# Performance work log

Hardware: AMD Instinct MI355X
Metric: run time of the kernel (lower is better)

The kernel has to match this reference:

```python
import jax, jax.numpy as jnp
import numpy as np

NUM_GRAPHS = 2048


def gcn_conv(x, W, b, edge, N):
    # PyG GCNConv: x' = D^{-1/2} (A + I) D^{-1/2} (x W) + b
    src, dst = edge[0], edge[1]
    loop = jnp.arange(N, dtype=src.dtype)
    src = jnp.concatenate([src, loop])
    dst = jnp.concatenate([dst, loop])
    h = x @ W  # [N, out]
    deg = jax.ops.segment_sum(jnp.ones(dst.shape, x.dtype), dst, num_segments=N)
    dinv = jnp.where(deg > 0, jax.lax.rsqrt(deg), 0.0)
    norm = dinv[src] * dinv[dst]  # [E+N]
    out = jax.ops.segment_sum(h[src] * norm[:, None], dst, num_segments=N)
    return out + b


def pool_max_mean(x, batch, G):
    mx = jax.ops.segment_max(x, batch, num_segments=G)
    mx = jnp.where(jnp.isfinite(mx), mx, 0.0)  # guard empty segments
    s = jax.ops.segment_sum(x, batch, num_segments=G)
    cnt = jax.ops.segment_sum(jnp.ones((x.shape[0],), x.dtype), batch, num_segments=G)
    mean = s / jnp.maximum(cnt, 1.0)[:, None]
    return mx, mean


def setup_inputs() -> dict:
    key = jax.random.key(0)
    ks = jax.random.split(key, 20)
    F, CE, SE, DD = 64, 64, 32, 128
    Nc, Ec, Ns, Es = 100000, 1250000, 100000, 1250000

    def glorot(k, shape):
        fan_in, fan_out = shape[0], shape[1]
        lim = np.sqrt(6.0 / (fan_in + fan_out)).astype(np.float32)
        return jax.random.uniform(k, shape, jnp.float32, -lim, lim)

    inp = {
        "c": jax.random.normal(ks[0], (Nc, F), jnp.float32),
        "c_edge": jax.random.randint(ks[1], (2, Ec), 0, Nc),
        "c_batch": jnp.sort(jax.random.randint(ks[2], (Nc,), 0, NUM_GRAPHS)),
        "s": jax.random.normal(ks[3], (Ns, F), jnp.float32),
        "s_edge": jax.random.randint(ks[4], (2, Es), 0, Ns),
        "s_batch": jnp.sort(jax.random.randint(ks[5], (Ns,), 0, NUM_GRAPHS)),
        "Wc0": glorot(ks[6], (F, CE)), "bc0": jnp.zeros((CE,), jnp.float32),
        "Wc1": glorot(ks[7], (CE, CE)), "bc1": jnp.zeros((CE,), jnp.float32),
        "Wc2": glorot(ks[8], (CE, CE)), "bc2": jnp.zeros((CE,), jnp.float32),
        "Ws0": glorot(ks[9], (F, SE)), "bs0": jnp.zeros((SE,), jnp.float32),
        "Ws1": glorot(ks[10], (SE, SE)), "bs1": jnp.zeros((SE,), jnp.float32),
        "Ws2": glorot(ks[11], (SE, SE)), "bs2": jnp.zeros((SE,), jnp.float32),
        "Wd": glorot(ks[12], ((CE + SE) * 2, DD)), "bd": jnp.zeros((DD,), jnp.float32),
        "Wo": glorot(ks[13], (DD, 1)), "bo": jnp.zeros((1,), jnp.float32),
    }
    return inp


def reference(c, c_edge, c_batch, s, s_edge, s_batch,
              Wc0, bc0, Wc1, bc1, Wc2, bc2,
              Ws0, bs0, Ws1, bs1, Ws2, bs2,
              Wd, bd, Wo, bo):
    Nc, Ns = c.shape[0], s.shape[0]
    cro = jax.nn.relu(gcn_conv(c, Wc0, bc0, c_edge, Nc))
    cro = jax.nn.relu(gcn_conv(cro, Wc1, bc1, c_edge, Nc))
    cro = jax.nn.relu(gcn_conv(cro, Wc2, bc2, c_edge, Nc))
    solv = jax.nn.relu(gcn_conv(s, Ws0, bs0, s_edge, Ns))
    solv = jax.nn.relu(gcn_conv(solv, Ws1, bs1, s_edge, Ns))
    solv = jax.nn.relu(gcn_conv(solv, Ws2, bs2, s_edge, Ns))
    c_mx, c_mean = pool_max_mean(cro, c_batch, NUM_GRAPHS)
    s_mx, s_mean = pool_max_mean(solv, s_batch, NUM_GRAPHS)
    embed = jnp.concatenate([c_mx, c_mean, s_mx, s_mean], axis=1)  # [G, 192]
    dense = jax.nn.relu(embed @ Wd + bd)
    out = dense @ Wo + bo  # [G, 1]
    return out, embed
```

## Files before the change

### kernel.cpp

```cpp
#include <hip/hip_runtime.h>
#include <hip/hip_fp16.h>
#include <math.h>


static inline int cdiv(int a, int b) { return (a + b - 1) / b; }

#define BUCKET_CAP 8192
#define P1_CHUNK   4096

typedef _Float16 v8h __attribute__((ext_vector_type(8)));
typedef float    v4f __attribute__((ext_vector_type(4)));

__global__ void zero_int(int* __restrict__ p, int n) {
    int i = blockIdx.x * blockDim.x + threadIdx.x;
    if (i < n) p[i] = 0;
}

__global__ __launch_bounds__(256) void p1_partition(const int* __restrict__ c_edge, int Ec,
                                                    const int* __restrict__ s_edge, int Es,
                                                    int Nc_pad, int Etot, int nbuck,
                                                    int* __restrict__ bucket_fill,
                                                    unsigned* __restrict__ pk) {
    __shared__ unsigned       wbuf[P1_CHUNK];
    __shared__ unsigned short bbuf[P1_CHUNK];
    __shared__ int            hist[512];
    int e0 = blockIdx.x * P1_CHUNK;
    int n  = Etot - e0;
    if (n > P1_CHUNK) n = P1_CHUNK;
    for (int i = threadIdx.x; i < nbuck; i += 256) hist[i] = 0;
    __syncthreads();
    for (int i = threadIdx.x; i < n; i += 256) {
        int e = e0 + i, src, g;
        if (e < Ec) { src = c_edge[e]; g = c_edge[Ec + e]; }
        else        { int e2 = e - Ec; src = s_edge[e2]; g = Nc_pad + s_edge[Es + e2]; }
        int b   = g >> 9;
        wbuf[i] = ((unsigned)(g & 511) << 17) | (unsigned)src;
        bbuf[i] = (unsigned short)b;
        atomicAdd(&hist[b], 1);
    }
    __syncthreads();
    for (int i = threadIdx.x; i < nbuck; i += 256) {
        int h = hist[i];
        hist[i] = h ? atomicAdd(&bucket_fill[i], h) : 0;
    }
    __syncthreads();
    for (int i = threadIdx.x; i < n; i += 256) {
        int b    = bbuf[i];
        int slot = atomicAdd(&hist[b], 1);
        if (slot < BUCKET_CAP) pk[(size_t)b * BUCKET_CAP + slot] = wbuf[i];
    }
}

__global__ __launch_bounds__(512) void p2_scanbuckets(const int* __restrict__ fill, int nbuck,
                                                      int* __restrict__ basearr,
                                                      int* __restrict__ off_all, int Ntot_pad, int Etot) {
    __shared__ int sh[512];
    int v = (threadIdx.x < nbuck) ? fill[threadIdx.x] : 0;
    sh[threadIdx.x] = v;
    __syncthreads();
    for (int ofs = 1; ofs < 512; ofs <<= 1) {
        int t = (threadIdx.x >= ofs) ? sh[threadIdx.x - ofs] : 0;
        __syncthreads();
        sh[threadIdx.x] += t;
        __syncthreads();
    }
    if (threadIdx.x < nbuck) basearr[threadIdx.x] = sh[threadIdx.x] - v;
    if (threadIdx.x == 0) off_all[Ntot_pad] = Etot;
}

__global__ __launch_bounds__(512) void p3_build(const unsigned* __restrict__ pk,
                                                const int* __restrict__ fillarr,
                                                const int* __restrict__ basearr,
                                                int* __restrict__ off_all,
                                                float* __restrict__ dinv,
                                                int* __restrict__ csr) {
    __shared__ int sh[512];
    int b    = blockIdx.x;
    int fill = fillarr[b];
    if (fill > BUCKET_CAP) fill = BUCKET_CAP;
    int base = basearr[b];
    const unsigned* reg = pk + (size_t)b * BUCKET_CAP;
    sh[threadIdx.x] = 0;
    __syncthreads();
    for (int i = threadIdx.x; i < fill; i += 512) atomicAdd(&sh[reg[i] >> 17], 1);
    __syncthreads();
    int cnt = sh[threadIdx.x];
    for (int ofs = 1; ofs < 512; ofs <<= 1) {
        int t = (threadIdx.x >= ofs) ? sh[threadIdx.x - ofs] : 0;
        __syncthreads();
        sh[threadIdx.x] += t;
        __syncthreads();
    }
    int excl = sh[threadIdx.x] - cnt;
    int node = b * 512 + threadIdx.x;
    off_all[node] = base + excl;
    dinv[node]    = rsqrtf((float)(cnt + 1));
    __syncthreads();
    sh[threadIdx.x] = excl;
    __syncthreads();
    for (int i = threadIdx.x; i < fill; i += 512) {
        unsigned w    = reg[i];
        int      slot = atomicAdd(&sh[w >> 17], 1);
        csr[base + slot] = (int)(w & 0x1FFFFu);
    }
}

template <int K, int M, typename TIN>
__device__ void gemm_mfma(int bid, const TIN* __restrict__ X, const float* __restrict__ W,
                          const float* __restrict__ dinv, __half* __restrict__ H, int N,
                          char* smem_) {
    constexpr int RB = 64;
    constexpr int KP = K + 8;
    constexpr int NT = M / 16;
    constexpr int KS = K / 32;
    _Float16* Xh = (_Float16*)smem_;
    _Float16* Wz = Xh + RB * KP;
    const int t    = threadIdx.x;
    const int row0 = bid * RB;

    constexpr int WENT = NT * KS * 64;
    for (int idx = t; idx < WENT; idx += 256) {
        int lane = idx & 63, rest = idx >> 6;
        int ks = rest % KS, ntl = rest / KS;
        int kbase = ks * 32 + (lane >> 4) * 8;
        int col   = ntl * 16 + (lane & 15);
        union { float4 f4; _Float16 h[8]; } u;
#pragma unroll
        for (int j = 0; j < 8; ++j) u.h[j] = (_Float16)W[(kbase + j) * M + col];
        *(float4*)(Wz + idx * 8) = u.f4;
    }
    if constexpr (sizeof(TIN) == 4) {
        constexpr int NI = RB * K / 4;
        for (int idx = t; idx < NI; idx += 256) {
            int row = idx / (K / 4), k4 = idx % (K / 4);
            int gr = row0 + row;
            float4 v = make_float4(0.f, 0.f, 0.f, 0.f);
            if (gr < N) v = *(const float4*)((const float*)X + (size_t)gr * K + k4 * 4);
            union { float2 f2; _Float16 h[4]; } u;
            u.h[0] = (_Float16)v.x; u.h[1] = (_Float16)v.y;
            u.h[2] = (_Float16)v.z; u.h[3] = (_Float16)v.w;
            *(float2*)(Xh + row * KP + k4 * 4) = u.f2;
        }
    } else {
        constexpr int NI = RB * K / 8;
        for (int idx = t; idx < NI; idx += 256) {
            int row = idx / (K / 8), k8 = idx % (K / 8);
            int gr = row0 + row;
            float4 v = make_float4(0.f, 0.f, 0.f, 0.f);
            if (gr < N) v = *(const float4*)((const __half*)X + (size_t)gr * K + k8 * 8);
            *(float4*)(Xh + row * KP + k8 * 8) = v;
        }
    }
    __syncthreads();

    const int wave = t >> 6, lane = t & 63;
    const int quad = lane >> 4, nl = lane & 15;
    const int rowA = wave * 16 + nl;

    v4f acc[NT];
#pragma unroll
    for (int i = 0; i < NT; ++i) acc[i] = (v4f){0.f, 0.f, 0.f, 0.f};

#pragma unroll
    for (int ks = 0; ks < KS; ++ks) {
        v8h a = *(const v8h*)(Xh + rowA * KP + ks * 32 + quad * 8);
#pragma unroll
        for (int ntl = 0; ntl < NT; ++ntl) {
            v8h b = *(const v8h*)(Wz + ((ntl * KS + ks) * 64 + lane) * 8);
            acc[ntl] = __builtin_amdgcn_mfma_f32_16x16x32_f16(a, b, acc[ntl], 0, 0, 0);
        }
    }

#pragma unroll
    for (int r = 0; r < 4; ++r) {
        int gr = row0 + wave * 16 + quad * 4 + r;
        if (gr < N) {
            float dv = dinv[gr];
#pragma unroll
            for (int ntl = 0; ntl < NT; ++ntl)
                H[(size_t)gr * M + ntl * 16 + nl] = __float2half(acc[ntl][r] * dv);
        }
    }
}

__device__ __forceinline__ float4 load4h(const float2* __restrict__ base, size_t idx) {
    float2 r = base[idx];
    union { float2 f2; __half2 h2[2]; } u;
    u.f2 = r;
    float2 a = __half22float2(u.h2[0]);
    float2 b = __half22float2(u.h2[1]);
    return make_float4(a.x, a.y, b.x, b.y);
}

__device__ __forceinline__ void load8h(const float4* __restrict__ base, size_t idx,
                                       float* __restrict__ o) {
    float4 r = base[idx];
    union { float4 f4; __half2 h2[4]; } u;
    u.f4 = r;
    float2 p0 = __half22float2(u.h2[0]);
    float2 p1 = __half22float2(u.h2[1]);
    float2 p2 = __half22float2(u.h2[2]);
    float2 p3 = __half22float2(u.h2[3]);
    o[0] = p0.x; o[1] = p0.y; o[2] = p1.x; o[3] = p1.y;
    o[4] = p2.x; o[5] = p2.y; o[6] = p3.x; o[7] = p3.y;
}

template <int MF>
__device__ void fused_agg_gemm(int bid, const __half* __restrict__ Hin,
                               const int* __restrict__ off_g, const int* __restrict__ csr,
                               const float* __restrict__ dinv_g, const float* __restrict__ b,
                               const float* __restrict__ W, __half* __restrict__ Hout,
                               int N, char* smem_) {
    constexpr int KP = MF + 8;
    constexpr int NT = MF / 16;
    constexpr int KS = MF / 32;
    _Float16* Xh = (_Float16*)smem_;
    _Float16* Wz = Xh + 64 * KP;
    const int t = threadIdx.x;

    constexpr int WENT = NT * KS * 64;
    for (int idx = t; idx < WENT; idx += 256) {
        int lane = idx & 63, rest = idx >> 6;
        int ks = rest % KS, ntl = rest / KS;
        int kbase = ks * 32 + (lane >> 4) * 8;
        int col   = ntl * 16 + (lane & 15);
        union { float4 f4; _Float16 h[8]; } u;
#pragma unroll
        for (int j = 0; j < 8; ++j) u.h[j] = (_Float16)W[(kbase + j) * MF + col];
        *(float4*)(Wz + idx * 8) = u.f4;
    }

    constexpr int L      = MF / 8;
    constexpr int NPW    = 64 / L;
    constexpr int PASSES = 64 / (4 * NPW);
    const int lane = t & 63, wave = t >> 6;
    const int fq = lane & (L - 1), sub = lane / L;
    const float4* H4 = (const float4*)Hin;
    const float4* b4 = (const float4*)b;
    float bb[8];
    {
        float4 b0 = b4[fq * 2], b1 = b4[fq * 2 + 1];
        bb[0] = b0.x; bb[1] = b0.y; bb[2] = b0.z; bb[3] = b0.w;
        bb[4] = b1.x; bb[5] = b1.y; bb[6] = b1.z; bb[7] = b1.w;
    }
#pragma unroll
    for (int pass = 0; pass < PASSES; ++pass) {
        int ln   = (pass * 4 + wave) * NPW + sub;
        int node = bid * 64 + ln;
        if (node < N) {
            int j0 = off_g[node], j1 = off_g[node + 1];
            float acc[8];
            load8h(H4, (size_t)node * L + fq, acc);
            int j = j0;
            for (; j + 8 <= j1; j += 8) {
                int s0 = csr[j],     s1 = csr[j + 1], s2 = csr[j + 2], s3 = csr[j + 3];
                int s4 = csr[j + 4], s5 = csr[j + 5], s6 = csr[j + 6], s7 = csr[j + 7];
                float a0[8], a1[8], a2[8], a3[8], a4[8], a5[8], a6[8], a7[8];
                load8h(H4, (size_t)s0 * L + fq, a0);
                load8h(H4, (size_t)s1 * L + fq, a1);
                load8h(H4, (size_t)s2 * L + fq, a2);
                load8h(H4, (size_t)s3 * L + fq, a3);
                load8h(H4, (size_t)s4 * L + fq, a4);
                load8h(H4, (size_t)s5 * L + fq, a5);
                load8h(H4, (size_t)s6 * L + fq, a6);
                load8h(H4, (size_t)s7 * L + fq, a7);
#pragma unroll
                for (int f = 0; f < 8; ++f) {
                    float g1 = ((a0[f] + a1[f]) + a2[f]) + a3[f];
                    float g2 = ((a4[f] + a5[f]) + a6[f]) + a7[f];
                    acc[f] += g1 + g2;
                }
            }
            for (; j + 4 <= j1; j += 4) {
                int s0 = csr[j], s1 = csr[j + 1], s2 = csr[j + 2], s3 = csr[j + 3];
                float a0[8], a1[8], a2[8], a3[8];
                load8h(H4, (size_t)s0 * L + fq, a0);
                load8h(H4, (size_t)s1 * L + fq, a1);
                load8h(H4, (size_t)s2 * L + fq, a2);
                load8h(H4, (size_t)s3 * L + fq, a3);
#pragma unroll
                for (int f = 0; f < 8; ++f)
                    acc[f] += ((a0[f] + a1[f]) + a2[f]) + a3[f];
            }
            for (; j < j1; ++j) {
                float a0[8];
                load8h(H4, (size_t)csr[j] * L + fq, a0);
#pragma unroll
                for (int f = 0; f < 8; ++f) acc[f] += a0[f];
            }
            float dv = dinv_g[node];
            union { float4 f4; __half2 h2[4]; } o;
#pragma unroll
            for (int p2 = 0; p2 < 4; ++p2) {
                float vx = dv * acc[2 * p2]     + bb[2 * p2];
                float vy = dv * acc[2 * p2 + 1] + bb[2 * p2 + 1];
                o.h2[p2] = __floats2half2_rn(vx > 0.f ? vx : 0.f, vy > 0.f ? vy : 0.f);
            }
            *(float4*)(Xh + ln * KP + fq * 8) = o.f4;
        } else {
            *(float4*)(Xh + ln * KP + fq * 8) = make_float4(0.f, 0.f, 0.f, 0.f);
        }
    }
    __syncthreads();

    const int quad = lane >> 4, nl = lane & 15;
    const int rowA = wave * 16 + nl;
    v4f acc2[NT];
#pragma unroll
    for (int i = 0; i < NT; ++i) acc2[i] = (v4f){0.f, 0.f, 0.f, 0.f};
#pragma unroll
    for (int ks = 0; ks < KS; ++ks) {
        v8h av = *(const v8h*)(Xh + rowA * KP + ks * 32 + quad * 8);
#pragma unroll
        for (int ntl = 0; ntl < NT; ++ntl) {
            v8h bv = *(const v8h*)(Wz + ((ntl * KS + ks) * 64 + lane) * 8);
            acc2[ntl] = __builtin_amdgcn_mfma_f32_16x16x32_f16(av, bv, acc2[ntl], 0, 0, 0);
        }
    }
#pragma unroll
    for (int r = 0; r < 4; ++r) {
        int gr = bid * 64 + wave * 16 + quad * 4 + r;
        if (gr < N) {
            float dv = dinv_g[gr];
#pragma unroll
            for (int ntl = 0; ntl < NT; ++ntl)
                Hout[(size_t)gr * MF + ntl * 16 + nl] = __float2half(acc2[ntl][r] * dv);
        }
    }
}

template <int M>
__device__ void agg_body(int bid, const __half* __restrict__ H,
                         const int* __restrict__ off_g,
                         const int* __restrict__ csr,
                         const float* __restrict__ dinv_g,
                         const float* __restrict__ b,
                         __half* __restrict__ out, int Nloc) {
    constexpr int L   = M / 4;
    constexpr int NPW = 64 / L;
    int lane = threadIdx.x & 63;
    int wave = threadIdx.x >> 6;
    int fq   = lane & (L - 1);
    int sub  = lane / L;
    int node = (bid * 4 + wave) * NPW + sub;
    if (node >= Nloc) return;
    const float2* H4 = (const float2*)H;
    int j0 = off_g[node], j1 = off_g[node + 1];
    float4 acc = load4h(H4, (size_t)node * L + fq);
    int j = j0;
    for (; j + 8 <= j1; j += 8) {
        int s0 = csr[j],     s1 = csr[j + 1], s2 = csr[j + 2], s3 = csr[j + 3];
        int s4 = csr[j + 4], s5 = csr[j + 5], s6 = csr[j + 6], s7 = csr[j + 7];
        float4 a0 = load4h(H4, (size_t)s0 * L + fq);
        float4 a1 = load4h(H4, (size_t)s1 * L + fq);
        float4 a2 = load4h(H4, (size_t)s2 * L + fq);
        float4 a3 = load4h(H4, (size_t)s3 * L + fq);
        float4 a4 = load4h(H4, (size_t)s4 * L + fq);
        float4 a5 = load4h(H4, (size_t)s5 * L + fq);
        float4 a6 = load4h(H4, (size_t)s6 * L + fq);
        float4 a7 = load4h(H4, (size_t)s7 * L + fq);
        acc.x += (a0.x + a1.x + a2.x + a3.x) + (a4.x + a5.x + a6.x + a7.x);
        acc.y += (a0.y + a1.y + a2.y + a3.y) + (a4.y + a5.y + a6.y + a7.y);
        acc.z += (a0.z + a1.z + a2.z + a3.z) + (a4.z + a5.z + a6.z + a7.z);
        acc.w += (a0.w + a1.w + a2.w + a3.w) + (a4.w + a5.w + a6.w + a7.w);
    }
    for (; j + 4 <= j1; j += 4) {
        int s0 = csr[j], s1 = csr[j + 1], s2 = csr[j + 2], s3 = csr[j + 3];
        float4 a0 = load4h(H4, (size_t)s0 * L + fq);
        float4 a1 = load4h(H4, (size_t)s1 * L + fq);
        float4 a2 = load4h(H4, (size_t)s2 * L + fq);
        float4 a3 = load4h(H4, (size_t)s3 * L + fq);
        acc.x += a0.x + a1.x + a2.x + a3.x;
        acc.y += a0.y + a1.y + a2.y + a3.y;
        acc.z += a0.z + a1.z + a2.z + a3.z;
        acc.w += a0.w + a1.w + a2.w + a3.w;
    }
    for (; j < j1; ++j) {
        float4 a = load4h(H4, (size_t)csr[j] * L + fq);
        acc.x += a.x; acc.y += a.y; acc.z += a.z; acc.w += a.w;
    }
    float  dv = dinv_g[node];
    float4 bb = ((const float4*)b)[fq];
    float  vx = dv * acc.x + bb.x;
    float  vy = dv * acc.y + bb.y;
    float  vz = dv * acc.z + bb.z;
    float  vw = dv * acc.w + bb.w;
    union { float2 f2; __half2 h2[2]; } o;
    o.h2[0] = __floats2half2_rn(vx > 0.f ? vx : 0.f, vy > 0.f ? vy : 0.f);
    o.h2[1] = __floats2half2_rn(vz > 0.f ? vz : 0.f, vw > 0.f ? vw : 0.f);
    ((float2*)out)[(size_t)node * L + fq] = o.f2;
}

__global__ __launch_bounds__(256) void gemmBoth0(const float* __restrict__ Xc, const float* __restrict__ Wc,
                                                 __half* __restrict__ cH, int Nc,
                                                 const float* __restrict__ Xs, const float* __restrict__ Ws,
                                                 __half* __restrict__ sH, int Ns,
                                                 const float* __restrict__ dinv_all, int Nc_pad, int nbC) {
    __shared__ __align__(16) char smem[17408];
    if (blockIdx.x < nbC) gemm_mfma<64, 64, float>(blockIdx.x, Xc, Wc, dinv_all, cH, Nc, smem);
    else                  gemm_mfma<64, 32, float>(blockIdx.x - nbC, Xs, Ws, dinv_all + Nc_pad, sH, Ns, smem);
}

__global__ __launch_bounds__(256) void fusedBoth(
        const __half* __restrict__ cHin, __half* __restrict__ cHout,
        const float* __restrict__ Wc, const float* __restrict__ bc,
        const __half* __restrict__ sHin, __half* __restrict__ sHout,
        const float* __restrict__ Ws, const float* __restrict__ bs,
        const int* __restrict__ off_all, const int* __restrict__ csr_all,
        const float* __restrict__ dinv_all,
        int Nc, int Ns, int Nc_pad, int nbC) {
    __shared__ __align__(16) char smem[17408];
    if (blockIdx.x < nbC)
        fused_agg_gemm<64>(blockIdx.x, cHin, off_all, csr_all, dinv_all, bc, Wc, cHout, Nc, smem);
    else
        fused_agg_gemm<32>(blockIdx.x - nbC, sHin, off_all + Nc_pad, csr_all,
                           dinv_all + Nc_pad, bs, Ws, sHout, Ns, smem);
}

__global__ __launch_bounds__(256) void aggBoth(const __half* __restrict__ cH, const __half* __restrict__ sH,
                                               const int* __restrict__ off_all, const int* __restrict__ csr_all,
                                               const float* __restrict__ dinv_all,
                                               const float* __restrict__ bc, const float* __restrict__ bs,
                                               __half* __restrict__ outc, __half* __restrict__ outs,
                                               int Nc, int Ns, int Nc_pad, int nbC) {
    if (blockIdx.x < nbC)
        agg_body<64>(blockIdx.x, cH, off_all, csr_all, dinv_all, bc, outc, Nc);
    else
        agg_body<32>(blockIdx.x - nbC, sH, off_all + Nc_pad, csr_all,
                     dinv_all + Nc_pad, bs, outs, Ns);
}

__device__ __forceinline__ int lbound(const int* __restrict__ a, int n, int key) {
    int lo = 0, hi = n;
    while (lo < hi) {
        int mid = (lo + hi) >> 1;
        if (a[mid] < key) lo = mid + 1; else hi = mid;
    }
    return lo;
}

__global__ __launch_bounds__(256) void poolDense(const __half* __restrict__ cX, const int* __restrict__ c_batch, int Nc,
                                                 const __half* __restrict__ sX, const int* __restrict__ s_batch, int Ns,
                                                 const float* __restrict__ Wd, const float* __restrict__ bd,
                                                 const float* __restrict__ Wo, const float* __restrict__ bo,
                                                 float* __restrict__ outv, float* __restrict__ embed) {
    __shared__ float e[192];
    __shared__ float red[2048];
    __shared__ float rs[128];
    int g = blockIdx.x, t = threadIdx.x;
    const float2* c4 = (const float2*)cX;
    const float2* s4 = (const float2*)sX;
    int clo = lbound(c_batch, Nc, g), chi = lbound(c_batch, Nc, g + 1);
    {
        int q = t & 15, grp = t >> 4;
        float mx0 = 0.f, mx1 = 0.f, mx2 = 0.f, mx3 = 0.f;
        float sm0 = 0.f, sm1 = 0.f, sm2 = 0.f, sm3 = 0.f;
        for (int i = clo + grp; i < chi; i += 16) {
            float4 v = load4h(c4, (size_t)i * 16 + q);
            mx0 = fmaxf(mx0, v.x); sm0 += v.x;
            mx1 = fmaxf(mx1, v.y); sm1 += v.y;
            mx2 = fmaxf(mx2, v.z); sm2 += v.z;
            mx3 = fmaxf(mx3, v.w); sm3 += v.w;
        }
        red[grp * 64 + q * 4 + 0]        = mx0;
        red[grp * 64 + q * 4 + 1]        = mx1;
        red[grp * 64 + q * 4 + 2]        = mx2;
        red[grp * 64 + q * 4 + 3]        = mx3;
        red[1024 + grp * 64 + q * 4 + 0] = sm0;
        red[1024 + grp * 64 + q * 4 + 1] = sm1;
        red[1024 + grp * 64 + q * 4 + 2] = sm2;
        red[1024 + grp * 64 + q * 4 + 3] = sm3;
    }
    __syncthreads();
    if (t < 64) {
        float m = red[t], s = red[1024 + t];
#pragma unroll
        for (int grp = 1; grp < 16; ++grp) {
            m = fmaxf(m, red[grp * 64 + t]);
            s += red[1024 + grp * 64 + t];
        }
        int cn = chi - clo;
        e[t]      = m;
        e[64 + t] = s / (float)(cn > 0 ? cn : 1);
    }
    __syncthreads();
    int slo = lbound(s_batch, Ns, g), shi = lbound(s_batch, Ns, g + 1);
    {
        int q = t & 7, grp = t >> 3;
        float mx0 = 0.f, mx1 = 0.f, mx2 = 0.f, mx3 = 0.f;
        float sm0 = 0.f, sm1 = 0.f, sm2 = 0.f, sm3 = 0.f;
        for (int i = slo + grp; i < shi; i += 32) {
            float4 v = load4h(s4, (size_t)i * 8 + q);
            mx0 = fmaxf(mx0, v.x); sm0 += v.x;
            mx1 = fmaxf(mx1, v.y); sm1 += v.y;
            mx2 = fmaxf(mx2, v.z); sm2 += v.z;
            mx3 = fmaxf(mx3, v.w); sm3 += v.w;
        }
        red[grp * 32 + q * 4 + 0]        = mx0;
        red[grp * 32 + q * 4 + 1]        = mx1;
        red[grp * 32 + q * 4 + 2]        = mx2;
        red[grp * 32 + q * 4 + 3]        = mx3;
        red[1024 + grp * 32 + q * 4 + 0] = sm0;
        red[1024 + grp * 32 + q * 4 + 1] = sm1;
        red[1024 + grp * 32 + q * 4 + 2] = sm2;
        red[1024 + grp * 32 + q * 4 + 3] = sm3;
    }
    __syncthreads();
    if (t < 32) {
        float m = red[t], s = red[1024 + t];
#pragma unroll
        for (int grp = 1; grp < 32; ++grp) {
            m = fmaxf(m, red[grp * 32 + t]);
            s += red[1024 + grp * 32 + t];
        }
        int cn = shi - slo;
        e[128 + t] = m;
        e[160 + t] = s / (float)(cn > 0 ? cn : 1);
    }
    __syncthreads();
    if (t < 192) embed[(size_t)g * 192 + t] = e[t];
    if (t < 128) {
        float acc = bd[t];
        for (int k = 0; k < 192; ++k) acc += e[k] * Wd[k * 128 + t];
        float d = acc > 0.f ? acc : 0.f;
        rs[t] = d * Wo[t];
    }
    __syncthreads();
    for (int ofs = 64; ofs > 0; ofs >>= 1) {
        if (t < ofs) rs[t] += rs[t + ofs];
        __syncthreads();
    }
    if (t == 0) outv[g] = rs[0] + bo[0];
}


extern "C" void kernel_launch(void* const* d_in, const int* in_sizes, int n_in,
                              void* d_out, int out_size, void* d_ws, size_t ws_size,
                              hipStream_t stream) {
    const float* c       = (const float*)d_in[0];
    const int*   c_edge  = (const int*)d_in[1];
    const int*   c_batch = (const int*)d_in[2];
    const float* s       = (const float*)d_in[3];
    const int*   s_edge  = (const int*)d_in[4];
    const int*   s_batch = (const int*)d_in[5];
    const float* Wc0 = (const float*)d_in[6],  *bc0 = (const float*)d_in[7];
    const float* Wc1 = (const float*)d_in[8],  *bc1 = (const float*)d_in[9];
    const float* Wc2 = (const float*)d_in[10], *bc2 = (const float*)d_in[11];
    const float* Ws0 = (const float*)d_in[12], *bs0 = (const float*)d_in[13];
    const float* Ws1 = (const float*)d_in[14], *bs1 = (const float*)d_in[15];
    const float* Ws2 = (const float*)d_in[16], *bs2 = (const float*)d_in[17];
    const float* Wd  = (const float*)d_in[18], *bd  = (const float*)d_in[19];
    const float* Wo  = (const float*)d_in[20], *bo  = (const float*)d_in[21];

    const int Nc = in_sizes[0] / 64;
    const int Ec = in_sizes[1] / 2;
    const int Ns = in_sizes[3] / 64;
    const int Es = in_sizes[4] / 2;
    const int G  = out_size / 193;
    const int Nc_pad   = cdiv(Nc, 512) * 512;
    const int Ns_pad   = cdiv(Ns, 512) * 512;
    const int Ntot_pad = Nc_pad + Ns_pad;
    const int Etot     = Ec + Es;
    const int nbuck    = Ntot_pad >> 9;

    char* p = (char*)d_ws;
    auto  alloc = [&](size_t bytes) -> void* {
        void* r = (void*)p;
        p += (bytes + 255) & ~(size_t)255;
        return r;
    };
    int*      bucket_fill = (int*)alloc(512 * 4);
    int*      bucket_base = (int*)alloc(512 * 4);
    unsigned* pk          = (unsigned*)alloc((size_t)nbuck * BUCKET_CAP * 4);
    int*      off_all     = (int*)alloc(((size_t)Ntot_pad + 1) * 4);
    int*      csr_all     = (int*)alloc((size_t)Etot * 4);
    float*    dinv_all    = (float*)alloc((size_t)Ntot_pad * 4);
    __half*   bufC        = (__half*)alloc((size_t)Nc * 64 * 2);
    __half*   bufS        = (__half*)alloc((size_t)Ns * 32 * 2);
    __half*   cHa         = (__half*)alloc((size_t)Nc * 64 * 2);
    __half*   cHb         = (__half*)alloc((size_t)Nc * 64 * 2);
    __half*   sHa         = (__half*)alloc((size_t)Ns * 32 * 2);
    __half*   sHb         = (__half*)alloc((size_t)Ns * 32 * 2);

    float* outv  = (float*)d_out;
    float* embed = outv + G;

    const int nbGmC = cdiv(Nc, 64), nbGmS = cdiv(Ns, 64);
    const int nbFC  = cdiv(Nc, 64), nbFS  = cdiv(Ns, 64);
    const int nbAgC = Nc_pad / 16,  nbAgS = Ns_pad / 32;

    zero_int<<<cdiv(nbuck, 256), 256, 0, stream>>>(bucket_fill, nbuck);
    p1_partition<<<cdiv(Etot, P1_CHUNK), 256, 0, stream>>>(c_edge, Ec, s_edge, Es,
                                                           Nc_pad, Etot, nbuck, bucket_fill, pk);
    p2_scanbuckets<<<1, 512, 0, stream>>>(bucket_fill, nbuck, bucket_base, off_all, Ntot_pad, Etot);
    p3_build<<<nbuck, 512, 0, stream>>>(pk, bucket_fill, bucket_base,
                                        off_all, dinv_all, csr_all);

    gemmBoth0<<<nbGmC + nbGmS, 256, 0, stream>>>(c, Wc0, cHa, Nc, s, Ws0, sHa, Ns,
                                                 dinv_all, Nc_pad, nbGmC);

    fusedBoth<<<nbFC + nbFS, 256, 0, stream>>>(cHa, cHb, Wc1, bc0, sHa, sHb, Ws1, bs0,
                                               off_all, csr_all, dinv_all,
                                               Nc, Ns, Nc_pad, nbFC);
    fusedBoth<<<nbFC + nbFS, 256, 0, stream>>>(cHb, cHa, Wc2, bc1, sHb, sHa, Ws2, bs1,
                                               off_all, csr_all, dinv_all,
                                               Nc, Ns, Nc_pad, nbFC);

    aggBoth<<<nbAgC + nbAgS, 256, 0, stream>>>(cHa, sHa, off_all, csr_all, dinv_all,
                                               bc2, bs2, bufC, bufS, Nc, Ns, Nc_pad, nbAgC);

    poolDense<<<G, 256, 0, stream>>>(bufC, c_batch, Nc, bufS, s_batch, Ns,
                                     Wd, bd, Wo, bo, outv, embed);
}
```

Measured before the change: 356.9 us.

## Shrink crystal fused tile to 32 rows and interleave crystal/solvent blocks

```diff
diff --git a/kernel.cpp b/kernel.cpp
--- a/kernel.cpp
+++ b/kernel.cpp
@@ -14,6 +14,15 @@
 __global__ void zero_int(int* __restrict__ p, int n) {
     int i = blockIdx.x * blockDim.x + threadIdx.x;
     if (i < n) p[i] = 0;
+}
+
+__device__ __forceinline__ bool split_grid(int bid, int nMaj, int nMin, int& idx) {
+    int T  = nMaj + nMin;
+    int g0 = (int)(((long long)bid * nMin) / T);
+    int g1 = (int)(((long long)(bid + 1) * nMin) / T);
+    if (g1 > g0) { idx = g0; return true; }
+    idx = bid - g0;
+    return false;
 }
 
 __global__ __launch_bounds__(256) void p1_partition(const int* __restrict__ c_edge, int Ec,
@@ -205,17 +214,19 @@
     o[4] = p2.x; o[5] = p2.y; o[6] = p3.x; o[7] = p3.y;
 }
 
-template <int MF>
+template <int MF, int RB>
 __device__ void fused_agg_gemm(int bid, const __half* __restrict__ Hin,
                                const int* __restrict__ off_g, const int* __restrict__ csr,
                                const float* __restrict__ dinv_g, const float* __restrict__ b,
                                const float* __restrict__ W, __half* __restrict__ Hout,
                                int N, char* smem_) {
-    constexpr int KP = MF + 8;
-    constexpr int NT = MF / 16;
-    constexpr int KS = MF / 32;
+    constexpr int KP  = MF + 8;
+    constexpr int NT  = MF / 16;
+    constexpr int KS  = MF / 32;
+    constexpr int RT  = RB / 16;
+    constexpr int TPW = RT * NT / 4;
     _Float16* Xh = (_Float16*)smem_;
-    _Float16* Wz = Xh + 64 * KP;
+    _Float16* Wz = Xh + RB * KP;
     const int t = threadIdx.x;
 
     constexpr int WENT = NT * KS * 64;
@@ -230,9 +241,9 @@
         *(float4*)(Wz + idx * 8) = u.f4;
     }
 
-    constexpr int L      = MF / 8;
-    constexpr int NPW    = 64 / L;
-    constexpr int PASSES = 64 / (4 * NPW);
+    constexpr int L   = MF / 8;
+    constexpr int NPW = 64 / L;
+    static_assert(4 * NPW == RB, "one gather pass");
     const int lane = t & 63, wave = t >> 6;
     const int fq = lane & (L - 1), sub = lane / L;
     const float4* H4 = (const float4*)Hin;
@@ -243,10 +254,9 @@
         bb[0] = b0.x; bb[1] = b0.y; bb[2] = b0.z; bb[3] = b0.w;
         bb[4] = b1.x; bb[5] = b1.y; bb[6] = b1.z; bb[7] = b1.w;
     }
-#pragma unroll
-    for (int pass = 0; pass < PASSES; ++pass) {
-        int ln   = (pass * 4 + wave) * NPW + sub;
-        int node = bid * 64 + ln;
+    {
+        int ln   = wave * NPW + sub;
+        int node = bid * RB + ln;
         if (node < N) {
             int j0 = off_g[node], j1 = off_g[node + 1];
             float acc[8];
@@ -304,27 +314,29 @@
     __syncthreads();
 
     const int quad = lane >> 4, nl = lane & 15;
-    const int rowA = wave * 16 + nl;
-    v4f acc2[NT];
-#pragma unroll
-    for (int i = 0; i < NT; ++i) acc2[i] = (v4f){0.f, 0.f, 0.f, 0.f};
+    const int rt   = (wave * TPW) / NT;
+    const int ntl0 = (wave * TPW) % NT;
+    const int rowA = rt * 16 + nl;
+    v4f acc2[TPW];
+#pragma unroll
+    for (int i = 0; i < TPW; ++i) acc2[i] = (v4f){0.f, 0.f, 0.f, 0.f};
 #pragma unroll
     for (int ks = 0; ks < KS; ++ks) {
         v8h av = *(const v8h*)(Xh + rowA * KP + ks * 32 + quad * 8);
 #pragma unroll
-        for (int ntl = 0; ntl < NT; ++ntl) {
-            v8h bv = *(const v8h*)(Wz + ((ntl * KS + ks) * 64 + lane) * 8);
-            acc2[ntl] = __builtin_amdgcn_mfma_f32_16x16x32_f16(av, bv, acc2[ntl], 0, 0, 0);
+        for (int k = 0; k < TPW; ++k) {
+            v8h bv = *(const v8h*)(Wz + (((ntl0 + k) * KS + ks) * 64 + lane) * 8);
+            acc2[k] = __builtin_amdgcn_mfma_f32_16x16x32_f16(av, bv, acc2[k], 0, 0, 0);
         }
     }
 #pragma unroll
     for (int r = 0; r < 4; ++r) {
-        int gr = bid * 64 + wave * 16 + quad * 4 + r;
+        int gr = bid * RB + rt * 16 + quad * 4 + r;
         if (gr < N) {
             float dv = dinv_g[gr];
 #pragma unroll
-            for (int ntl = 0; ntl < NT; ++ntl)
-                Hout[(size_t)gr * MF + ntl * 16 + nl] = __float2half(acc2[ntl][r] * dv);
+            for (int k = 0; k < TPW; ++k)
+                Hout[(size_t)gr * MF + (ntl0 + k) * 16 + nl] = __float2half(acc2[k][r] * dv);
         }
     }
 }
@@ -408,13 +420,14 @@
         const float* __restrict__ Ws, const float* __restrict__ bs,
         const int* __restrict__ off_all, const int* __restrict__ csr_all,
         const float* __restrict__ dinv_all,
-        int Nc, int Ns, int Nc_pad, int nbC) {
-    __shared__ __align__(16) char smem[17408];
-    if (blockIdx.x < nbC)
-        fused_agg_gemm<64>(blockIdx.x, cHin, off_all, csr_all, dinv_all, bc, Wc, cHout, Nc, smem);
+        int Nc, int Ns, int Nc_pad, int nbC, int nbS) {
+    __shared__ __align__(16) char smem[12800];
+    int idx;
+    if (split_grid(blockIdx.x, nbC, nbS, idx))
+        fused_agg_gemm<32, 64>(idx, sHin, off_all + Nc_pad, csr_all,
+                               dinv_all + Nc_pad, bs, Ws, sHout, Ns, smem);
     else
-        fused_agg_gemm<32>(blockIdx.x - nbC, sHin, off_all + Nc_pad, csr_all,
-                           dinv_all + Nc_pad, bs, Ws, sHout, Ns, smem);
+        fused_agg_gemm<64, 32>(idx, cHin, off_all, csr_all, dinv_all, bc, Wc, cHout, Nc, smem);
 }
 
 __global__ __launch_bounds__(256) void aggBoth(const __half* __restrict__ cH, const __half* __restrict__ sH,
@@ -586,7 +599,7 @@
     float* embed = outv + G;
 
     const int nbGmC = cdiv(Nc, 64), nbGmS = cdiv(Ns, 64);
-    const int nbFC  = cdiv(Nc, 64), nbFS  = cdiv(Ns, 64);
+    const int nbFC  = cdiv(Nc, 32), nbFS  = cdiv(Ns, 64);
     const int nbAgC = Nc_pad / 16,  nbAgS = Ns_pad / 32;
 
     zero_int<<<cdiv(nbuck, 256), 256, 0, stream>>>(bucket_fill, nbuck);
@@ -601,10 +614,10 @@
 
     fusedBoth<<<nbFC + nbFS, 256, 0, stream>>>(cHa, cHb, Wc1, bc0, sHa, sHb, Ws1, bs0,
                                                off_all, csr_all, dinv_all,
-                                               Nc, Ns, Nc_pad, nbFC);
+                                               Nc, Ns, Nc_pad, nbFC, nbFS);
     fusedBoth<<<nbFC + nbFS, 256, 0, stream>>>(cHb, cHa, Wc2, bc1, sHb, sHa, Ws2, bs1,
                                                off_all, csr_all, dinv_all,
-                                               Nc, Ns, Nc_pad, nbFC);
+                                               Nc, Ns, Nc_pad, nbFC, nbFS);
 
     aggBoth<<<nbAgC + nbAgS, 256, 0, stream>>>(cHa, sHa, off_all, csr_all, dinv_all,
                                                bc2, bs2, bufC, bufS, Nc, Ns, Nc_pad, nbAgC);
```

Result: slower. 373.1 us (+4.6%).

## Co-schedule edge partitioning with first GEMM and fold bucket scan into build

Applied to the files above, without the earlier changes.

```diff
diff --git a/kernel.cpp b/kernel.cpp
--- a/kernel.cpp
+++ b/kernel.cpp
@@ -6,7 +6,7 @@
 static inline int cdiv(int a, int b) { return (a + b - 1) / b; }
 
 #define BUCKET_CAP 8192
-#define P1_CHUNK   4096
+#define P1_CHUNK   2048
 
 typedef _Float16 v8h __attribute__((ext_vector_type(8)));
 typedef float    v4f __attribute__((ext_vector_type(4)));
@@ -16,15 +16,24 @@
     if (i < n) p[i] = 0;
 }
 
-__global__ __launch_bounds__(256) void p1_partition(const int* __restrict__ c_edge, int Ec,
-                                                    const int* __restrict__ s_edge, int Es,
-                                                    int Nc_pad, int Etot, int nbuck,
-                                                    int* __restrict__ bucket_fill,
-                                                    unsigned* __restrict__ pk) {
-    __shared__ unsigned       wbuf[P1_CHUNK];
-    __shared__ unsigned short bbuf[P1_CHUNK];
-    __shared__ int            hist[512];
-    int e0 = blockIdx.x * P1_CHUNK;
+__device__ __forceinline__ bool split_grid(int bid, int nMaj, int nMin, int& idx) {
+    int T  = nMaj + nMin;
+    int g0 = (int)(((long long)bid * nMin) / T);
+    int g1 = (int)(((long long)(bid + 1) * nMin) / T);
+    if (g1 > g0) { idx = g0; return true; }
+    idx = bid - g0;
+    return false;
+}
+
+__device__ void p1_body(int bid, const int* __restrict__ c_edge, int Ec,
+                        const int* __restrict__ s_edge, int Es,
+                        int Nc_pad, int Etot, int nbuck,
+                        int* __restrict__ bucket_fill,
+                        unsigned* __restrict__ pk, char* smem) {
+    unsigned*       wbuf = (unsigned*)smem;
+    unsigned short* bbuf = (unsigned short*)(smem + 8192);
+    int*            hist = (int*)(smem + 12288);
+    int e0 = bid * P1_CHUNK;
     int n  = Etot - e0;
     if (n > P1_CHUNK) n = P1_CHUNK;
     for (int i = threadIdx.x; i < nbuck; i += 256) hist[i] = 0;
@@ -51,34 +60,26 @@
     }
 }
 
-__global__ __launch_bounds__(512) void p2_scanbuckets(const int* __restrict__ fill, int nbuck,
-                                                      int* __restrict__ basearr,
-                                                      int* __restrict__ off_all, int Ntot_pad, int Etot) {
-    __shared__ int sh[512];
-    int v = (threadIdx.x < nbuck) ? fill[threadIdx.x] : 0;
-    sh[threadIdx.x] = v;
-    __syncthreads();
-    for (int ofs = 1; ofs < 512; ofs <<= 1) {
-        int t = (threadIdx.x >= ofs) ? sh[threadIdx.x - ofs] : 0;
-        __syncthreads();
-        sh[threadIdx.x] += t;
-        __syncthreads();
-    }
-    if (threadIdx.x < nbuck) basearr[threadIdx.x] = sh[threadIdx.x] - v;
-    if (threadIdx.x == 0) off_all[Ntot_pad] = Etot;
-}
-
 __global__ __launch_bounds__(512) void p3_build(const unsigned* __restrict__ pk,
-                                                const int* __restrict__ fillarr,
-                                                const int* __restrict__ basearr,
+                                                const int* __restrict__ fillarr, int nbuck,
                                                 int* __restrict__ off_all,
                                                 float* __restrict__ dinv,
-                                                int* __restrict__ csr) {
+                                                int* __restrict__ csr,
+                                                int Ntot_pad, int Etot) {
     __shared__ int sh[512];
-    int b    = blockIdx.x;
+    __shared__ int fsc[512];
+    int b = blockIdx.x;
+    fsc[threadIdx.x] = (threadIdx.x < nbuck) ? fillarr[threadIdx.x] : 0;
+    __syncthreads();
+    for (int ofs = 1; ofs < 512; ofs <<= 1) {
+        int t = (threadIdx.x >= ofs) ? fsc[threadIdx.x - ofs] : 0;
+        __syncthreads();
+        fsc[threadIdx.x] += t;
+        __syncthreads();
+    }
+    int base = (b > 0) ? fsc[b - 1] : 0;
     int fill = fillarr[b];
     if (fill > BUCKET_CAP) fill = BUCKET_CAP;
-    int base = basearr[b];
     const unsigned* reg = pk + (size_t)b * BUCKET_CAP;
     sh[threadIdx.x] = 0;
     __syncthreads();
@@ -95,6 +96,7 @@
     int node = b * 512 + threadIdx.x;
     off_all[node] = base + excl;
     dinv[node]    = rsqrtf((float)(cnt + 1));
+    if (b == 0 && threadIdx.x == 0) off_all[Ntot_pad] = Etot;
     __syncthreads();
     sh[threadIdx.x] = excl;
     __syncthreads();
@@ -107,8 +109,7 @@
 
 template <int K, int M, typename TIN>
 __device__ void gemm_mfma(int bid, const TIN* __restrict__ X, const float* __restrict__ W,
-                          const float* __restrict__ dinv, __half* __restrict__ H, int N,
-                          char* smem_) {
+                          __half* __restrict__ H, int N, char* smem_) {
     constexpr int RB = 64;
     constexpr int KP = K + 8;
     constexpr int NT = M / 16;
@@ -129,7 +130,7 @@
         for (int j = 0; j < 8; ++j) u.h[j] = (_Float16)W[(kbase + j) * M + col];
         *(float4*)(Wz + idx * 8) = u.f4;
     }
-    if constexpr (sizeof(TIN) == 4) {
+    {
         constexpr int NI = RB * K / 4;
         for (int idx = t; idx < NI; idx += 256) {
             int row = idx / (K / 4), k4 = idx % (K / 4);
@@ -141,15 +142,6 @@
             u.h[2] = (_Float16)v.z; u.h[3] = (_Float16)v.w;
             *(float2*)(Xh + row * KP + k4 * 4) = u.f2;
         }
-    } else {
-        constexpr int NI = RB * K / 8;
-        for (int idx = t; idx < NI; idx += 256) {
-            int row = idx / (K / 8), k8 = idx % (K / 8);
-            int gr = row0 + row;
-            float4 v = make_float4(0.f, 0.f, 0.f, 0.f);
-            if (gr < N) v = *(const float4*)((const __half*)X + (size_t)gr * K + k8 * 8);
-            *(float4*)(Xh + row * KP + k8 * 8) = v;
-        }
     }
     __syncthreads();
 
@@ -175,10 +167,9 @@
     for (int r = 0; r < 4; ++r) {
         int gr = row0 + wave * 16 + quad * 4 + r;
         if (gr < N) {
-            float dv = dinv[gr];
 #pragma unroll
             for (int ntl = 0; ntl < NT; ++ntl)
-                H[(size_t)gr * M + ntl * 16 + nl] = __float2half(acc[ntl][r] * dv);
+                H[(size_t)gr * M + ntl * 16 + nl] = __float2half(acc[ntl][r]);
         }
     }
 }
@@ -205,7 +196,7 @@
     o[4] = p2.x; o[5] = p2.y; o[6] = p3.x; o[7] = p3.y;
 }
 
-template <int MF>
+template <int MF, bool SRCSCALE>
 __device__ void fused_agg_gemm(int bid, const __half* __restrict__ Hin,
                                const int* __restrict__ off_g, const int* __restrict__ csr,
                                const float* __restrict__ dinv_g, const float* __restrict__ b,
@@ -251,6 +242,11 @@
             int j0 = off_g[node], j1 = off_g[node + 1];
             float acc[8];
             load8h(H4, (size_t)node * L + fq, acc);
+            if constexpr (SRCSCALE) {
+                float dvs = dinv_g[node];
+#pragma unroll
+                for (int f = 0; f < 8; ++f) acc[f] *= dvs;
+            }
             int j = j0;
             for (; j + 8 <= j1; j += 8) {
                 int s0 = csr[j],     s1 = csr[j + 1], s2 = csr[j + 2], s3 = csr[j + 3];
@@ -264,11 +260,22 @@
                 load8h(H4, (size_t)s5 * L + fq, a5);
                 load8h(H4, (size_t)s6 * L + fq, a6);
                 load8h(H4, (size_t)s7 * L + fq, a7);
-#pragma unroll
-                for (int f = 0; f < 8; ++f) {
-                    float g1 = ((a0[f] + a1[f]) + a2[f]) + a3[f];
-                    float g2 = ((a4[f] + a5[f]) + a6[f]) + a7[f];
-                    acc[f] += g1 + g2;
+                if constexpr (SRCSCALE) {
+                    float d0 = dinv_g[s0], d1 = dinv_g[s1], d2 = dinv_g[s2], d3 = dinv_g[s3];
+                    float d4 = dinv_g[s4], d5 = dinv_g[s5], d6 = dinv_g[s6], d7 = dinv_g[s7];
+#pragma unroll
+                    for (int f = 0; f < 8; ++f) {
+                        float g1 = fmaf(a0[f], d0, fmaf(a1[f], d1, fmaf(a2[f], d2, a3[f] * d3)));
+                        float g2 = fmaf(a4[f], d4, fmaf(a5[f], d5, fmaf(a6[f], d6, a7[f] * d7)));
+                        acc[f] += g1 + g2;
+                    }
+                } else {
+#pragma unroll
+                    for (int f = 0; f < 8; ++f) {
+                        float g1 = ((a0[f] + a1[f]) + a2[f]) + a3[f];
+                        float g2 = ((a4[f] + a5[f]) + a6[f]) + a7[f];
+                        acc[f] += g1 + g2;
+                    }
                 }
             }
             for (; j + 4 <= j1; j += 4) {
@@ -278,15 +285,29 @@
                 load8h(H4, (size_t)s1 * L + fq, a1);
                 load8h(H4, (size_t)s2 * L + fq, a2);
                 load8h(H4, (size_t)s3 * L + fq, a3);
-#pragma unroll
-                for (int f = 0; f < 8; ++f)
-                    acc[f] += ((a0[f] + a1[f]) + a2[f]) + a3[f];
+                if constexpr (SRCSCALE) {
+                    float d0 = dinv_g[s0], d1 = dinv_g[s1], d2 = dinv_g[s2], d3 = dinv_g[s3];
+#pragma unroll
+                    for (int f = 0; f < 8; ++f)
+                        acc[f] += fmaf(a0[f], d0, fmaf(a1[f], d1, fmaf(a2[f], d2, a3[f] * d3)));
+                } else {
+#pragma unroll
+                    for (int f = 0; f < 8; ++f)
+                        acc[f] += ((a0[f] + a1[f]) + a2[f]) + a3[f];
+                }
             }
             for (; j < j1; ++j) {
+                int s0 = csr[j];
                 float a0[8];
-                load8h(H4, (size_t)csr[j] * L + fq, a0);
-#pragma unroll
-                for (int f = 0; f < 8; ++f) acc[f] += a0[f];
+                load8h(H4, (size_t)s0 * L + fq, a0);
+                if constexpr (SRCSCALE) {
+                    float d0 = dinv_g[s0];
+#pragma unroll
+                    for (int f = 0; f < 8; ++f) acc[f] = fmaf(a0[f], d0, acc[f]);
+                } else {
+#pragma unroll
+                    for (int f = 0; f < 8; ++f) acc[f] += a0[f];
+                }
             }
             float dv = dinv_g[node];
             union { float4 f4; __half2 h2[4]; } o;
@@ -391,16 +412,25 @@
     ((float2*)out)[(size_t)node * L + fq] = o.f2;
 }
 
-__global__ __launch_bounds__(256) void gemmBoth0(const float* __restrict__ Xc, const float* __restrict__ Wc,
-                                                 __half* __restrict__ cH, int Nc,
-                                                 const float* __restrict__ Xs, const float* __restrict__ Ws,
-                                                 __half* __restrict__ sH, int Ns,
-                                                 const float* __restrict__ dinv_all, int Nc_pad, int nbC) {
+__global__ __launch_bounds__(256) void p1_gemm0(
+        const int* __restrict__ c_edge, int Ec, const int* __restrict__ s_edge, int Es,
+        int Nc_pad, int Etot, int nbuck,
+        int* __restrict__ bucket_fill, unsigned* __restrict__ pk,
+        const float* __restrict__ Xc, const float* __restrict__ Wc0, __half* __restrict__ cH, int Nc,
+        const float* __restrict__ Xs, const float* __restrict__ Ws0, __half* __restrict__ sH, int Ns,
+        int nP1, int nGemC, int nGemS) {
     __shared__ __align__(16) char smem[17408];
-    if (blockIdx.x < nbC) gemm_mfma<64, 64, float>(blockIdx.x, Xc, Wc, dinv_all, cH, Nc, smem);
-    else                  gemm_mfma<64, 32, float>(blockIdx.x - nbC, Xs, Ws, dinv_all + Nc_pad, sH, Ns, smem);
-}
-
+    int idx;
+    if (split_grid(blockIdx.x, nGemC + nGemS, nP1, idx)) {
+        p1_body(idx, c_edge, Ec, s_edge, Es, Nc_pad, Etot, nbuck, bucket_fill, pk, smem);
+    } else if (idx < nGemC) {
+        gemm_mfma<64, 64, float>(idx, Xc, Wc0, cH, Nc, smem);
+    } else {
+        gemm_mfma<64, 32, float>(idx - nGemC, Xs, Ws0, sH, Ns, smem);
+    }
+}
+
+template <bool SRCSCALE>
 __global__ __launch_bounds__(256) void fusedBoth(
         const __half* __restrict__ cHin, __half* __restrict__ cHout,
         const float* __restrict__ Wc, const float* __restrict__ bc,
@@ -411,10 +441,10 @@
         int Nc, int Ns, int Nc_pad, int nbC) {
     __shared__ __align__(16) char smem[17408];
     if (blockIdx.x < nbC)
-        fused_agg_gemm<64>(blockIdx.x, cHin, off_all, csr_all, dinv_all, bc, Wc, cHout, Nc, smem);
+        fused_agg_gemm<64, SRCSCALE>(blockIdx.x, cHin, off_all, csr_all, dinv_all, bc, Wc, cHout, Nc, smem);
     else
-        fused_agg_gemm<32>(blockIdx.x - nbC, sHin, off_all + Nc_pad, csr_all,
-                           dinv_all + Nc_pad, bs, Ws, sHout, Ns, smem);
+        fused_agg_gemm<32, SRCSCALE>(blockIdx.x - nbC, sHin, off_all + Nc_pad, csr_all,
+                                     dinv_all + Nc_pad, bs, Ws, sHout, Ns, smem);
 }
 
 __global__ __launch_bounds__(256) void aggBoth(const __half* __restrict__ cH, const __half* __restrict__ sH,
@@ -570,7 +600,6 @@
         return r;
     };
     int*      bucket_fill = (int*)alloc(512 * 4);
-    int*      bucket_base = (int*)alloc(512 * 4);
     unsigned* pk          = (unsigned*)alloc((size_t)nbuck * BUCKET_CAP * 4);
     int*      off_all     = (int*)alloc(((size_t)Ntot_pad + 1) * 4);
     int*      csr_all     = (int*)alloc((size_t)Etot * 4);
@@ -588,23 +617,23 @@
     const int nbGmC = cdiv(Nc, 64), nbGmS = cdiv(Ns, 64);
     const int nbFC  = cdiv(Nc, 64), nbFS  = cdiv(Ns, 64);
     const int nbAgC = Nc_pad / 16,  nbAgS = Ns_pad / 32;
+    const int nP1   = cdiv(Etot, P1_CHUNK);
 
     zero_int<<<cdiv(nbuck, 256), 256, 0, stream>>>(bucket_fill, nbuck);
-    p1_partition<<<cdiv(Etot, P1_CHUNK), 256, 0, stream>>>(c_edge, Ec, s_edge, Es,
-                                                           Nc_pad, Etot, nbuck, bucket_fill, pk);
-    p2_scanbuckets<<<1, 512, 0, stream>>>(bucket_fill, nbuck, bucket_base, off_all, Ntot_pad, Etot);
-    p3_build<<<nbuck, 512, 0, stream>>>(pk, bucket_fill, bucket_base,
-                                        off_all, dinv_all, csr_all);
-
-    gemmBoth0<<<nbGmC + nbGmS, 256, 0, stream>>>(c, Wc0, cHa, Nc, s, Ws0, sHa, Ns,
-                                                 dinv_all, Nc_pad, nbGmC);
-
-    fusedBoth<<<nbFC + nbFS, 256, 0, stream>>>(cHa, cHb, Wc1, bc0, sHa, sHb, Ws1, bs0,
-                                               off_all, csr_all, dinv_all,
-                                               Nc, Ns, Nc_pad, nbFC);
-    fusedBoth<<<nbFC + nbFS, 256, 0, stream>>>(cHb, cHa, Wc2, bc1, sHb, sHa, Ws2, bs1,
-                                               off_all, csr_all, dinv_all,
-                                               Nc, Ns, Nc_pad, nbFC);
+
+    p1_gemm0<<<nP1 + nbGmC + nbGmS, 256, 0, stream>>>(
+        c_edge, Ec, s_edge, Es, Nc_pad, Etot, nbuck, bucket_fill, pk,
+        c, Wc0, cHa, Nc, s, Ws0, sHa, Ns, nP1, nbGmC, nbGmS);
+
+    p3_build<<<nbuck, 512, 0, stream>>>(pk, bucket_fill, nbuck,
+                                        off_all, dinv_all, csr_all, Ntot_pad, Etot);
+
+    fusedBoth<true><<<nbFC + nbFS, 256, 0, stream>>>(
+        cHa, cHb, Wc1, bc0, sHa, sHb, Ws1, bs0,
+        off_all, csr_all, dinv_all, Nc, Ns, Nc_pad, nbFC);
+    fusedBoth<false><<<nbFC + nbFS, 256, 0, stream>>>(
+        cHb, cHa, Wc2, bc1, sHb, sHa, Ws2, bs1,
+        off_all, csr_all, dinv_all, Nc, Ns, Nc_pad, nbFC);
 
     aggBoth<<<nbAgC + nbAgS, 256, 0, stream>>>(cHa, sHa, off_all, csr_all, dinv_all,
                                                bc2, bs2, bufC, bufS, Nc, Ns, Nc_pad, nbAgC);
```

Measured after the change: 361.4 us. About the same (+1.3%).
